# Kernel tuning notes

Measured on AMD Instinct MI355X. Metric: run time of the kernel, lower is better.

The kernel has to match this reference:

```python
import jax, jax.numpy as jnp
import numpy as np


def setup_inputs() -> dict:
    key = jax.random.key(0)
    k1, k2, k3 = jax.random.split(key, 3)
    B, L, Z, C = 2048, 128, 256, 256  # predictive_steps == L
    z = jax.random.normal(k1, (B, L, Z), dtype=jnp.float32)
    c = jax.random.normal(k2, (B, L, C), dtype=jnp.float32)
    # original inits trans to zeros; use small random values so output is non-trivial
    trans = jax.random.normal(k3, (L, Z, C), dtype=jnp.float32) * 0.02
    return {"z": z, "c": c, "trans": trans}


def reference(z, c, trans):
    # Original per-t: r[:, t] = (z[:, t] @ trans[t] @ c[:, t].T).sum(-1)
    # Row-sum of the (b x b) score matrix equals projecting z onto trans[t] @ sum_b c[b, t],
    # which is exactly the same math without materializing the (b x b) intermediate.
    csum = jnp.sum(c, axis=0)                      # (L, C)
    v = jnp.einsum('lzc,lc->lz', trans, csum)      # (L, Z)
    r = jnp.einsum('blz,lz->bl', z, v)             # (B, L)
    return jnp.exp(r)
```

## Files before the change

kernel.cpp:

```cpp
#include <hip/hip_runtime.h>
#include <math.h>

#define NB 2048
#define NL 128
#define NZ 256
#define NC 256
#define BCHUNK 128
#define NCHUNK (NB / BCHUNK)

__global__ __launch_bounds__(256) void csum_partial_kernel(const float* __restrict__ c,
                                                           float* __restrict__ partial) {
    const int l     = blockIdx.x;
    const int chunk = blockIdx.y;
    const int lane  = threadIdx.x & 63;
    const int w     = threadIdx.x >> 6;

    const size_t b0 = (size_t)chunk * BCHUNK + (size_t)w * (BCHUNK / 4);
    const float4* base = (const float4*)(c + (b0 * NL + l) * NC) + lane;

    float4 acc = {0.f, 0.f, 0.f, 0.f};
#pragma unroll 8
    for (int i = 0; i < BCHUNK / 4; ++i) {
        float4 t = base[(size_t)i * (NL * NC / 4)];
        acc.x += t.x; acc.y += t.y; acc.z += t.z; acc.w += t.w;
    }

    __shared__ float4 s4[256];
    s4[threadIdx.x] = acc;
    __syncthreads();

    if (threadIdx.x < 64) {
        float4 a = s4[threadIdx.x];
        float4 b = s4[64 + threadIdx.x];
        float4 d = s4[128 + threadIdx.x];
        float4 e = s4[192 + threadIdx.x];
        float4 r;
        r.x = a.x + b.x + d.x + e.x;
        r.y = a.y + b.y + d.y + e.y;
        r.z = a.z + b.z + d.z + e.z;
        r.w = a.w + b.w + d.w + e.w;
        ((float4*)(partial + ((size_t)chunk * NL + l) * NC))[threadIdx.x] = r;
    }
}

__global__ __launch_bounds__(256) void csum_reduce_kernel(const float* __restrict__ partial,
                                                          float* __restrict__ csum) {
    const int l = blockIdx.x;
    const int t = threadIdx.x;
    float s = 0.f;
#pragma unroll
    for (int k = 0; k < NCHUNK; ++k)
        s += partial[((size_t)k * NL + l) * NC + t];
    csum[l * NC + t] = s;
}

__global__ __launch_bounds__(256) void v_kernel(const float* __restrict__ trans,
                                                const float* __restrict__ csum,
                                                float* __restrict__ v) {
    const int lane = threadIdx.x & 63;
    const int wv   = threadIdx.x >> 6;
    const int o0   = (blockIdx.x * 4 + wv) * 4;
    const int l    = o0 >> 8;

    float4 s = ((const float4*)(csum + l * NC))[lane];

    float acc[4];
#pragma unroll
    for (int k = 0; k < 4; ++k) {
        float4 t = ((const float4*)(trans + (size_t)(o0 + k) * NC))[lane];
        acc[k] = t.x * s.x + t.y * s.y + t.z * s.z + t.w * s.w;
    }
#pragma unroll
    for (int m = 32; m >= 1; m >>= 1) {
#pragma unroll
        for (int k = 0; k < 4; ++k) acc[k] += __shfl_xor(acc[k], m, 64);
    }
    if (lane == 0) *((float4*)(v + o0)) = make_float4(acc[0], acc[1], acc[2], acc[3]);
}

__global__ __launch_bounds__(256) void r_kernel(const float* __restrict__ z,
                                                const float* __restrict__ v,
                                                float* __restrict__ out) {
    const int lane = threadIdx.x & 63;
    const int wv   = threadIdx.x >> 6;
    const int gw   = blockIdx.x * 4 + wv;

#pragma unroll
    for (int jj = 0; jj < 4; ++jj) {
        const int o0 = gw * 16 + jj * 4;
        float acc[4];
#pragma unroll
        for (int k = 0; k < 4; ++k) {
            const int o = o0 + k;
            const int l = o & (NL - 1);
            float4 zf = ((const float4*)(z + (size_t)o * NZ))[lane];
            float4 vf = ((const float4*)(v + l * NZ))[lane];
            acc[k] = zf.x * vf.x + zf.y * vf.y + zf.z * vf.z + zf.w * vf.w;
        }
#pragma unroll
        for (int m = 32; m >= 1; m >>= 1) {
#pragma unroll
            for (int k = 0; k < 4; ++k) acc[k] += __shfl_xor(acc[k], m, 64);
        }
        if (lane == 0) {
            *((float4*)(out + o0)) = make_float4(expf(fminf(acc[0], 88.f)),
                                                 expf(fminf(acc[1], 88.f)),
                                                 expf(fminf(acc[2], 88.f)),
                                                 expf(fminf(acc[3], 88.f)));
        }
    }
}

extern "C" void kernel_launch(void* const* d_in, const int* in_sizes, int n_in,
                              void* d_out, int out_size, void* d_ws, size_t ws_size,
                              hipStream_t stream) {
    const float* z     = (const float*)d_in[0];
    const float* c     = (const float*)d_in[1];
    const float* trans = (const float*)d_in[2];
    float* out = (float*)d_out;

    float* partial = (float*)d_ws;
    float* csum    = partial + (size_t)NCHUNK * NL * NC;
    float* v       = csum + NL * NC;

    dim3 gA(NL, NCHUNK);
    csum_partial_kernel<<<gA, 256, 0, stream>>>(c, partial);

    csum_reduce_kernel<<<NL, 256, 0, stream>>>(partial, csum);

    v_kernel<<<(NL * NZ) / 16, 256, 0, stream>>>(trans, csum, v);

    r_kernel<<<(NB * NL) / 64, 256, 0, stream>>>(z, v, out);
}
```

Measured before the change: 528.2 us.

## Fuse four kernels into one cooperative persistent kernel with grid syncs

Replaces the four separate launches (partial column sums, reduction, trans projection, z dot-product with exp) with a single cooperative kernel of 1024 blocks that loops over the work and separates the phases with grid-wide barriers. The csum reduction is folded into the v phase, where each wave re-reads the 16 partial chunks itself. The aim is to remove launch overhead and the inter-kernel drain gaps. In exchange it adds grid-sync costs, redundant partial-sum reads, and a fixed grid that may reduce memory-level parallelism in the bandwidth-bound z pass.

```diff
diff --git a/kernel.cpp b/kernel.cpp
--- a/kernel.cpp
+++ b/kernel.cpp
@@ -1,5 +1,8 @@
 #include <hip/hip_runtime.h>
+#include <hip/hip_cooperative_groups.h>
 #include <math.h>
+
+namespace cg = cooperative_groups;
 
 #define NB 2048
 #define NL 128
@@ -7,94 +10,94 @@
 #define NC 256
 #define BCHUNK 128
 #define NCHUNK (NB / BCHUNK)
+#define GRID 1024
 
-__global__ __launch_bounds__(256) void csum_partial_kernel(const float* __restrict__ c,
-                                                           float* __restrict__ partial) {
-    const int l     = blockIdx.x;
-    const int chunk = blockIdx.y;
-    const int lane  = threadIdx.x & 63;
-    const int w     = threadIdx.x >> 6;
+__global__ __launch_bounds__(256, 4) void fused_all(const float* __restrict__ z,
+                                                    const float* __restrict__ c,
+                                                    const float* __restrict__ trans,
+                                                    float* __restrict__ out,
+                                                    float* __restrict__ ws) {
+    float* partial = ws;
+    float* v       = ws + (size_t)NCHUNK * NL * NC;
 
-    const size_t b0 = (size_t)chunk * BCHUNK + (size_t)w * (BCHUNK / 4);
-    const float4* base = (const float4*)(c + (b0 * NL + l) * NC) + lane;
+    const int tid  = threadIdx.x;
+    const int lane = tid & 63;
+    const int wv   = tid >> 6;
+    const int bid  = blockIdx.x;
 
-    float4 acc = {0.f, 0.f, 0.f, 0.f};
+    cg::grid_group grid = cg::this_grid();
+
+    __shared__ float4 s4[256];
+
+#pragma unroll
+    for (int it = 0; it < 2; ++it) {
+        const int u     = bid + it * GRID;
+        const int l     = u & (NL - 1);
+        const int chunk = u >> 7;
+        const size_t b0 = (size_t)chunk * BCHUNK + (size_t)wv * (BCHUNK / 4);
+        const float4* base = (const float4*)(c + (b0 * NL + l) * NC) + lane;
+        float4 acc = {0.f, 0.f, 0.f, 0.f};
 #pragma unroll 8
-    for (int i = 0; i < BCHUNK / 4; ++i) {
-        float4 t = base[(size_t)i * (NL * NC / 4)];
-        acc.x += t.x; acc.y += t.y; acc.z += t.z; acc.w += t.w;
+        for (int i = 0; i < BCHUNK / 4; ++i) {
+            float4 t = base[(size_t)i * (NL * NC / 4)];
+            acc.x += t.x; acc.y += t.y; acc.z += t.z; acc.w += t.w;
+        }
+        s4[tid] = acc;
+        __syncthreads();
+        if (tid < 64) {
+            float4 a = s4[tid], b = s4[64 + tid], d = s4[128 + tid], e = s4[192 + tid];
+            float4 r;
+            r.x = a.x + b.x + d.x + e.x;
+            r.y = a.y + b.y + d.y + e.y;
+            r.z = a.z + b.z + d.z + e.z;
+            r.w = a.w + b.w + d.w + e.w;
+            ((float4*)(partial + ((size_t)chunk * NL + l) * NC))[tid] = r;
+        }
+        __syncthreads();
     }
 
-    __shared__ float4 s4[256];
-    s4[threadIdx.x] = acc;
-    __syncthreads();
-
-    if (threadIdx.x < 64) {
-        float4 a = s4[threadIdx.x];
-        float4 b = s4[64 + threadIdx.x];
-        float4 d = s4[128 + threadIdx.x];
-        float4 e = s4[192 + threadIdx.x];
-        float4 r;
-        r.x = a.x + b.x + d.x + e.x;
-        r.y = a.y + b.y + d.y + e.y;
-        r.z = a.z + b.z + d.z + e.z;
-        r.w = a.w + b.w + d.w + e.w;
-        ((float4*)(partial + ((size_t)chunk * NL + l) * NC))[threadIdx.x] = r;
-    }
-}
-
-__global__ __launch_bounds__(256) void csum_reduce_kernel(const float* __restrict__ partial,
-                                                          float* __restrict__ csum) {
-    const int l = blockIdx.x;
-    const int t = threadIdx.x;
-    float s = 0.f;
-#pragma unroll
-    for (int k = 0; k < NCHUNK; ++k)
-        s += partial[((size_t)k * NL + l) * NC + t];
-    csum[l * NC + t] = s;
-}
-
-__global__ __launch_bounds__(256) void v_kernel(const float* __restrict__ trans,
-                                                const float* __restrict__ csum,
-                                                float* __restrict__ v) {
-    const int lane = threadIdx.x & 63;
-    const int wv   = threadIdx.x >> 6;
-    const int o0   = (blockIdx.x * 4 + wv) * 4;
-    const int l    = o0 >> 8;
-
-    float4 s = ((const float4*)(csum + l * NC))[lane];
-
-    float acc[4];
-#pragma unroll
-    for (int k = 0; k < 4; ++k) {
-        float4 t = ((const float4*)(trans + (size_t)(o0 + k) * NC))[lane];
-        acc[k] = t.x * s.x + t.y * s.y + t.z * s.z + t.w * s.w;
-    }
-#pragma unroll
-    for (int m = 32; m >= 1; m >>= 1) {
-#pragma unroll
-        for (int k = 0; k < 4; ++k) acc[k] += __shfl_xor(acc[k], m, 64);
-    }
-    if (lane == 0) *((float4*)(v + o0)) = make_float4(acc[0], acc[1], acc[2], acc[3]);
-}
-
-__global__ __launch_bounds__(256) void r_kernel(const float* __restrict__ z,
-                                                const float* __restrict__ v,
-                                                float* __restrict__ out) {
-    const int lane = threadIdx.x & 63;
-    const int wv   = threadIdx.x >> 6;
-    const int gw   = blockIdx.x * 4 + wv;
+    grid.sync();
 
 #pragma unroll
-    for (int jj = 0; jj < 4; ++jj) {
-        const int o0 = gw * 16 + jj * 4;
+    for (int it = 0; it < 2; ++it) {
+        const int g  = bid + it * GRID;
+        const int o0 = (g * 4 + wv) * 4;
+        const int l  = o0 >> 8;
+
+        float4 s = {0.f, 0.f, 0.f, 0.f};
+#pragma unroll
+        for (int k = 0; k < NCHUNK; ++k) {
+            float4 p = ((const float4*)(partial + ((size_t)k * NL + l) * NC))[lane];
+            s.x += p.x; s.y += p.y; s.z += p.z; s.w += p.w;
+        }
+
+        float acc[4];
+#pragma unroll
+        for (int k = 0; k < 4; ++k) {
+            float4 t = ((const float4*)(trans + (size_t)(o0 + k) * NC))[lane];
+            acc[k] = t.x * s.x + t.y * s.y + t.z * s.z + t.w * s.w;
+        }
+#pragma unroll
+        for (int m = 32; m >= 1; m >>= 1) {
+#pragma unroll
+            for (int k = 0; k < 4; ++k) acc[k] += __shfl_xor(acc[k], m, 64);
+        }
+        if (lane == 0) *((float4*)(v + o0)) = make_float4(acc[0], acc[1], acc[2], acc[3]);
+    }
+
+    grid.sync();
+
+    const int gw = bid * 4 + wv;
+#pragma unroll
+    for (int jj = 0; jj < 16; ++jj) {
+        const int o0 = gw * 64 + jj * 4;
         float acc[4];
 #pragma unroll
         for (int k = 0; k < 4; ++k) {
             const int o = o0 + k;
             const int l = o & (NL - 1);
             float4 zf = ((const float4*)(z + (size_t)o * NZ))[lane];
-            float4 vf = ((const float4*)(v + l * NZ))[lane];
+            float4 vf = ((const float4*)(v + (size_t)l * NZ))[lane];
             acc[k] = zf.x * vf.x + zf.y * vf.y + zf.z * vf.z + zf.w * vf.w;
         }
 #pragma unroll
@@ -118,17 +121,8 @@
     const float* c     = (const float*)d_in[1];
     const float* trans = (const float*)d_in[2];
     float* out = (float*)d_out;
+    float* ws  = (float*)d_ws;
 
-    float* partial = (float*)d_ws;
-    float* csum    = partial + (size_t)NCHUNK * NL * NC;
-    float* v       = csum + NL * NC;
-
-    dim3 gA(NL, NCHUNK);
-    csum_partial_kernel<<<gA, 256, 0, stream>>>(c, partial);
-
-    csum_reduce_kernel<<<NL, 256, 0, stream>>>(partial, csum);
-
-    v_kernel<<<(NL * NZ) / 16, 256, 0, stream>>>(trans, csum, v);
-
-    r_kernel<<<(NB * NL) / 64, 256, 0, stream>>>(z, v, out);
+    void* args[] = {(void*)&z, (void*)&c, (void*)&trans, (void*)&out, (void*)&ws};
+    hipLaunchCooperativeKernel((void*)fused_all, dim3(GRID), dim3(256), args, 0, stream);
 }
```

Result: slower. 779.4 us (+47.6%).

## Restructure csum reduction so each block reads contiguous 8KB rows of c

Applied to the files above, without the earlier changes.

The first stage of the batch-sum of c is reorganised. Each block now takes 8 batch rows and 32 contiguous l rows, so every wave streams contiguous 1KB rows instead of using strided single-row loads. This gives 256 partial sums per l, written to a larger workspace (32 MB). A second kernel reduces those partials with four waves per l. The aim is better DRAM access locality and more parallelism in the first pass, at the cost of more partial-sum traffic and a heavier second pass.

```diff
diff --git a/kernel.cpp b/kernel.cpp
--- a/kernel.cpp
+++ b/kernel.cpp
@@ -5,53 +5,69 @@
 #define NL 128
 #define NZ 256
 #define NC 256
-#define BCHUNK 128
-#define NCHUNK (NB / BCHUNK)
+
+#define BCH 8
+#define NCB (NB / BCH)
+#define LR 32
+#define NLR (NL / LR)
 
 __global__ __launch_bounds__(256) void csum_partial_kernel(const float* __restrict__ c,
                                                            float* __restrict__ partial) {
-    const int l     = blockIdx.x;
-    const int chunk = blockIdx.y;
-    const int lane  = threadIdx.x & 63;
-    const int w     = threadIdx.x >> 6;
+    const int cb   = blockIdx.x;
+    const int l0   = blockIdx.y * LR;
+    const int lane = threadIdx.x & 63;
+    const int wv   = threadIdx.x >> 6;
 
-    const size_t b0 = (size_t)chunk * BCHUNK + (size_t)w * (BCHUNK / 4);
-    const float4* base = (const float4*)(c + (b0 * NL + l) * NC) + lane;
+    const int b0 = cb * BCH;
+    const int lw = l0 + wv * 8;
+
+    float4 acc[8];
+#pragma unroll
+    for (int s = 0; s < 8; ++s) acc[s] = make_float4(0.f, 0.f, 0.f, 0.f);
+
+#pragma unroll 2
+    for (int b = 0; b < BCH; ++b) {
+        const float4* base = (const float4*)(c + ((size_t)(b0 + b) * NL + lw) * NC) + lane;
+#pragma unroll
+        for (int s = 0; s < 8; ++s) {
+            float4 t = base[(size_t)s * (NC / 4)];
+            acc[s].x += t.x; acc[s].y += t.y; acc[s].z += t.z; acc[s].w += t.w;
+        }
+    }
+
+#pragma unroll
+    for (int s = 0; s < 8; ++s) {
+        ((float4*)(partial + ((size_t)(lw + s) * NCB + cb) * NC))[lane] = acc[s];
+    }
+}
+
+__global__ __launch_bounds__(256) void csum_reduce_kernel(const float* __restrict__ partial,
+                                                          float* __restrict__ csum) {
+    const int l    = blockIdx.x;
+    const int lane = threadIdx.x & 63;
+    const int wv   = threadIdx.x >> 6;
 
     float4 acc = {0.f, 0.f, 0.f, 0.f};
+    const float4* base = (const float4*)(partial + ((size_t)l * NCB + wv * 64) * NC) + lane;
 #pragma unroll 8
-    for (int i = 0; i < BCHUNK / 4; ++i) {
-        float4 t = base[(size_t)i * (NL * NC / 4)];
+    for (int k = 0; k < 64; ++k) {
+        float4 t = base[(size_t)k * (NC / 4)];
         acc.x += t.x; acc.y += t.y; acc.z += t.z; acc.w += t.w;
     }
 
     __shared__ float4 s4[256];
     s4[threadIdx.x] = acc;
     __syncthreads();
-
     if (threadIdx.x < 64) {
-        float4 a = s4[threadIdx.x];
-        float4 b = s4[64 + threadIdx.x];
-        float4 d = s4[128 + threadIdx.x];
-        float4 e = s4[192 + threadIdx.x];
+        float4 a = s4[threadIdx.x], b = s4[64 + threadIdx.x],
+               d = s4[128 + threadIdx.x], e = s4[192 + threadIdx.x];
         float4 r;
         r.x = a.x + b.x + d.x + e.x;
         r.y = a.y + b.y + d.y + e.y;
         r.z = a.z + b.z + d.z + e.z;
         r.w = a.w + b.w + d.w + e.w;
-        ((float4*)(partial + ((size_t)chunk * NL + l) * NC))[threadIdx.x] = r;
+        ((float4*)(csum + (size_t)l * NC))[threadIdx.x] = r;
     }
-}
-
-__global__ __launch_bounds__(256) void csum_reduce_kernel(const float* __restrict__ partial,
-                                                          float* __restrict__ csum) {
-    const int l = blockIdx.x;
-    const int t = threadIdx.x;
-    float s = 0.f;
-#pragma unroll
-    for (int k = 0; k < NCHUNK; ++k)
-        s += partial[((size_t)k * NL + l) * NC + t];
-    csum[l * NC + t] = s;
 }
 
 __global__ __launch_bounds__(256) void v_kernel(const float* __restrict__ trans,
@@ -120,11 +136,10 @@
     float* out = (float*)d_out;
 
     float* partial = (float*)d_ws;
-    float* csum    = partial + (size_t)NCHUNK * NL * NC;
-    float* v       = csum + NL * NC;
+    float* csum    = partial + (size_t)NL * NCB * NC;
+    float* v       = csum + (size_t)NL * NC;
 
-    dim3 gA(NL, NCHUNK);
-    csum_partial_kernel<<<gA, 256, 0, stream>>>(c, partial);
+    csum_partial_kernel<<<dim3(NCB, NLR), 256, 0, stream>>>(c, partial);
 
     csum_reduce_kernel<<<NL, 256, 0, stream>>>(partial, csum);
 
```

New measurement: 536.3 us. About the same (+1.5%).
